# Performance work log

Hardware: AMD Instinct MI355X
Metric: run time of the kernel (lower is better)

Reference implementation:

```python
import jax, jax.numpy as jnp
import numpy as np

N_NODES = 40000
N_EDGES = 640000
HIDDEN = 128


def setup_inputs() -> dict:
    key = jax.random.key(0)
    k1, k2, k3, k4 = jax.random.split(key, 4)
    x = jax.random.normal(k1, (N_NODES, HIDDEN), dtype=jnp.float32)
    edge_index = jax.random.randint(k2, (2, N_EDGES), 0, N_NODES, dtype=jnp.int64)
    # nn.Linear(2*hidden, 1): weight [1, 2*hidden], bias [1]
    bound = 1.0 / np.sqrt(2 * HIDDEN)
    att_w = jax.random.uniform(k3, (1, 2 * HIDDEN), minval=-bound, maxval=bound, dtype=jnp.float32)
    att_b = jax.random.uniform(k4, (1,), minval=-bound, maxval=bound, dtype=jnp.float32)
    eps = jnp.array([0.1], dtype=jnp.float32)
    return {"x": x, "edge_index": edge_index, "att_w": att_w, "att_b": att_b, "eps": eps}


def reference(x, edge_index, att_w, att_b, eps):
    d = x.shape[1]
    row, col = edge_index[0], edge_index[1]
    x_i = x[row]                               # [E, d]
    x_j = x[col]                               # [E, d]
    # att(cat([x_i, x_j])) == x_i @ w_i + x_j @ w_j + b  (avoids materializing concat)
    w = att_w[0]                               # [2d]
    logits = x_i @ w[:d] + x_j @ w[d:] + att_b[0]   # [E]
    alpha = jnp.tanh(logits)
    messages = alpha[:, None] * x_i            # [E, d]
    out = jax.ops.segment_sum(messages, col, num_segments=x.shape[0])  # scatter_add over col
    e = eps[0]
    return e * x + (1.0 - e) * out
```

## Files before the change

kernel.cpp:

```cpp
#include <hip/hip_runtime.h>
#include <hip/hip_fp16.h>
#include <math.h>


#define NHID 128
#define NNODES 40000
#define NEDGES 640000
#define CAP 64

__global__ __launch_bounds__(256) void node_pre_kernel(
    const float* __restrict__ x,
    const float* __restrict__ att_w,
    const float* __restrict__ att_b,
    float* __restrict__ s1,
    float* __restrict__ s2,
    int* __restrict__ cursor) {
    int gid = blockIdx.x * 256 + threadIdx.x;
    if (gid < NNODES) cursor[gid] = 0;

    int node = blockIdx.x * 4 + (threadIdx.x >> 6);
    int lane = threadIdx.x & 63;
    if (node >= NNODES) return;

    float2 xv = ((const float2*)(x + (size_t)node * NHID))[lane];
    float2 w1 = ((const float2*)att_w)[lane];
    float2 w2 = ((const float2*)(att_w + NHID))[lane];

    float p1 = xv.x * w1.x + xv.y * w1.y;
    float p2 = xv.x * w2.x + xv.y * w2.y;
#pragma unroll
    for (int off = 32; off > 0; off >>= 1) {
        p1 += __shfl_down(p1, off, 64);
        p2 += __shfl_down(p2, off, 64);
    }
    if (lane == 0) {
        s1[node] = p1;
        s2[node] = p2 + att_b[0];
    }
}

__global__ __launch_bounds__(256) void bucket_kernel(
    const int* __restrict__ ei,
    const float* __restrict__ s1,
    const float* __restrict__ s2,
    const float* __restrict__ eps,
    int* __restrict__ cursor,
    unsigned* __restrict__ buck) {
    int e = blockIdx.x * 256 + threadIdx.x;
    if (e >= NEDGES) return;
    int r = ei[e];
    int c = ei[NEDGES + e];
    float a = (1.0f - eps[0]) * tanhf(s1[r] + s2[c]);
    int pos = atomicAdd(&cursor[c], 1);
    if (pos < CAP) {
        unsigned short hb = __half_as_ushort(__float2half_rn(a));
        buck[(size_t)c * CAP + pos] = ((unsigned)r << 16) | (unsigned)hb;
    }
}

__global__ __launch_bounds__(256) void gather_kernel(
    const float* __restrict__ x,
    const float* __restrict__ eps,
    const int* __restrict__ cursor,
    const unsigned* __restrict__ buck,
    float* __restrict__ out) {
    int node = blockIdx.x * 4 + (threadIdx.x >> 6);
    int lane = threadIdx.x & 63;
    if (node >= NNODES) return;

    int cnt = cursor[node];
    cnt = (cnt < CAP) ? cnt : CAP;

    unsigned pk = (lane < cnt) ? buck[(size_t)node * CAP + lane] : 0u;

    float2 xv = ((const float2*)(x + (size_t)node * NHID))[lane];
    float e = eps[0];
    float2 acc;
    acc.x = e * xv.x;
    acc.y = e * xv.y;

    int j = 0;
    for (; j + 4 <= cnt; j += 4) {
        unsigned p0 = __shfl(pk, j + 0, 64);
        unsigned p1 = __shfl(pk, j + 1, 64);
        unsigned p2 = __shfl(pk, j + 2, 64);
        unsigned p3 = __shfl(pk, j + 3, 64);
        float2 v0 = ((const float2*)(x + (size_t)(p0 >> 16) * NHID))[lane];
        float2 v1 = ((const float2*)(x + (size_t)(p1 >> 16) * NHID))[lane];
        float2 v2 = ((const float2*)(x + (size_t)(p2 >> 16) * NHID))[lane];
        float2 v3 = ((const float2*)(x + (size_t)(p3 >> 16) * NHID))[lane];
        float a0 = __half2float(__ushort_as_half((unsigned short)(p0 & 0xffffu)));
        float a1 = __half2float(__ushort_as_half((unsigned short)(p1 & 0xffffu)));
        float a2 = __half2float(__ushort_as_half((unsigned short)(p2 & 0xffffu)));
        float a3 = __half2float(__ushort_as_half((unsigned short)(p3 & 0xffffu)));
        acc.x += a0 * v0.x; acc.y += a0 * v0.y;
        acc.x += a1 * v1.x; acc.y += a1 * v1.y;
        acc.x += a2 * v2.x; acc.y += a2 * v2.y;
        acc.x += a3 * v3.x; acc.y += a3 * v3.y;
    }
    for (; j < cnt; j++) {
        unsigned p = __shfl(pk, j, 64);
        float2 v = ((const float2*)(x + (size_t)(p >> 16) * NHID))[lane];
        float a = __half2float(__ushort_as_half((unsigned short)(p & 0xffffu)));
        acc.x += a * v.x;
        acc.y += a * v.y;
    }
    ((float2*)(out + (size_t)node * NHID))[lane] = acc;
}

extern "C" void kernel_launch(void* const* d_in, const int* in_sizes, int n_in,
                              void* d_out, int out_size, void* d_ws, size_t ws_size,
                              hipStream_t stream) {
    const float* x     = (const float*)d_in[0];
    const int*   ei    = (const int*)d_in[1];
    const float* att_w = (const float*)d_in[2];
    const float* att_b = (const float*)d_in[3];
    const float* eps   = (const float*)d_in[4];
    float* out = (float*)d_out;

    float*    s1     = (float*)d_ws;
    float*    s2     = s1 + NNODES;
    int*      cursor = (int*)(s2 + NNODES);
    unsigned* buck   = (unsigned*)(cursor + NNODES);

    node_pre_kernel<<<NNODES / 4, 256, 0, stream>>>(
        x, att_w, att_b, s1, s2, cursor);
    bucket_kernel<<<(NEDGES + 255) / 256, 256, 0, stream>>>(
        ei, s1, s2, eps, cursor, buck);
    gather_kernel<<<NNODES / 4, 256, 0, stream>>>(
        x, eps, cursor, buck, out);
}
```

Measured before the change: 162.1 us.

## Gather fp16 copy of x, defer tanh to gather, pad atomic counters

The pre-pass now writes an fp16 copy of x, and the gather kernel reads neighbour rows from that copy, halving the bytes of the random row gathers. The attention coefficient is no longer computed in the bucket kernel. Buckets hold only 16-bit row indices, and the gather kernel computes tanh per lane from s1/s2 before broadcasting it with shuffles. Per-node counters are spaced 16 ints apart to spread the atomics across cache lines. This adds fp16 rounding of neighbour features, and the 16-bit row index cannot represent node ids above 65535.

```diff
diff --git a/kernel.cpp b/kernel.cpp
--- a/kernel.cpp
+++ b/kernel.cpp
@@ -7,6 +7,7 @@
 #define NNODES 40000
 #define NEDGES 640000
 #define CAP 64
+#define CSTRIDE 16
 
 __global__ __launch_bounds__(256) void node_pre_kernel(
     const float* __restrict__ x,
@@ -14,9 +15,10 @@
     const float* __restrict__ att_b,
     float* __restrict__ s1,
     float* __restrict__ s2,
+    __half* __restrict__ xh,
     int* __restrict__ cursor) {
     int gid = blockIdx.x * 256 + threadIdx.x;
-    if (gid < NNODES) cursor[gid] = 0;
+    if (gid < NNODES * CSTRIDE) cursor[gid] = 0;
 
     int node = blockIdx.x * 4 + (threadIdx.x >> 6);
     int lane = threadIdx.x & 63;
@@ -25,6 +27,11 @@
     float2 xv = ((const float2*)(x + (size_t)node * NHID))[lane];
     float2 w1 = ((const float2*)att_w)[lane];
     float2 w2 = ((const float2*)(att_w + NHID))[lane];
+
+    __half2 hv;
+    hv.x = __float2half_rn(xv.x);
+    hv.y = __float2half_rn(xv.y);
+    ((__half2*)(xh + (size_t)node * NHID))[lane] = hv;
 
     float p1 = xv.x * w1.x + xv.y * w1.y;
     float p2 = xv.x * w2.x + xv.y * w2.y;
@@ -41,67 +48,67 @@
 
 __global__ __launch_bounds__(256) void bucket_kernel(
     const int* __restrict__ ei,
-    const float* __restrict__ s1,
-    const float* __restrict__ s2,
-    const float* __restrict__ eps,
     int* __restrict__ cursor,
-    unsigned* __restrict__ buck) {
+    unsigned short* __restrict__ buck) {
     int e = blockIdx.x * 256 + threadIdx.x;
     if (e >= NEDGES) return;
     int r = ei[e];
     int c = ei[NEDGES + e];
-    float a = (1.0f - eps[0]) * tanhf(s1[r] + s2[c]);
-    int pos = atomicAdd(&cursor[c], 1);
+    int pos = atomicAdd(&cursor[c * CSTRIDE], 1);
     if (pos < CAP) {
-        unsigned short hb = __half_as_ushort(__float2half_rn(a));
-        buck[(size_t)c * CAP + pos] = ((unsigned)r << 16) | (unsigned)hb;
+        buck[(size_t)c * CAP + pos] = (unsigned short)r;
     }
 }
 
 __global__ __launch_bounds__(256) void gather_kernel(
     const float* __restrict__ x,
+    const __half* __restrict__ xh,
+    const float* __restrict__ s1,
+    const float* __restrict__ s2,
     const float* __restrict__ eps,
     const int* __restrict__ cursor,
-    const unsigned* __restrict__ buck,
+    const unsigned short* __restrict__ buck,
     float* __restrict__ out) {
     int node = blockIdx.x * 4 + (threadIdx.x >> 6);
     int lane = threadIdx.x & 63;
     if (node >= NNODES) return;
 
-    int cnt = cursor[node];
+    int cnt = cursor[node * CSTRIDE];
     cnt = (cnt < CAP) ? cnt : CAP;
 
-    unsigned pk = (lane < cnt) ? buck[(size_t)node * CAP + lane] : 0u;
+    float e = eps[0];
+    float coef = 1.0f - e;
+    float s2n = s2[node];
+
+    int   r_l = (lane < cnt) ? (int)buck[(size_t)node * CAP + lane] : 0;
+    float a_l = (lane < cnt) ? coef * tanhf(s1[r_l] + s2n) : 0.0f;
 
     float2 xv = ((const float2*)(x + (size_t)node * NHID))[lane];
-    float e = eps[0];
     float2 acc;
     acc.x = e * xv.x;
     acc.y = e * xv.y;
 
     int j = 0;
     for (; j + 4 <= cnt; j += 4) {
-        unsigned p0 = __shfl(pk, j + 0, 64);
-        unsigned p1 = __shfl(pk, j + 1, 64);
-        unsigned p2 = __shfl(pk, j + 2, 64);
-        unsigned p3 = __shfl(pk, j + 3, 64);
-        float2 v0 = ((const float2*)(x + (size_t)(p0 >> 16) * NHID))[lane];
-        float2 v1 = ((const float2*)(x + (size_t)(p1 >> 16) * NHID))[lane];
-        float2 v2 = ((const float2*)(x + (size_t)(p2 >> 16) * NHID))[lane];
-        float2 v3 = ((const float2*)(x + (size_t)(p3 >> 16) * NHID))[lane];
-        float a0 = __half2float(__ushort_as_half((unsigned short)(p0 & 0xffffu)));
-        float a1 = __half2float(__ushort_as_half((unsigned short)(p1 & 0xffffu)));
-        float a2 = __half2float(__ushort_as_half((unsigned short)(p2 & 0xffffu)));
-        float a3 = __half2float(__ushort_as_half((unsigned short)(p3 & 0xffffu)));
+        int   r0 = __shfl(r_l, j + 0, 64), r1 = __shfl(r_l, j + 1, 64);
+        int   r2 = __shfl(r_l, j + 2, 64), r3 = __shfl(r_l, j + 3, 64);
+        float a0 = __shfl(a_l, j + 0, 64), a1 = __shfl(a_l, j + 1, 64);
+        float a2 = __shfl(a_l, j + 2, 64), a3 = __shfl(a_l, j + 3, 64);
+        __half2 h0 = ((const __half2*)(xh + (size_t)r0 * NHID))[lane];
+        __half2 h1 = ((const __half2*)(xh + (size_t)r1 * NHID))[lane];
+        __half2 h2 = ((const __half2*)(xh + (size_t)r2 * NHID))[lane];
+        __half2 h3 = ((const __half2*)(xh + (size_t)r3 * NHID))[lane];
+        float2 v0 = __half22float2(h0), v1 = __half22float2(h1);
+        float2 v2 = __half22float2(h2), v3 = __half22float2(h3);
         acc.x += a0 * v0.x; acc.y += a0 * v0.y;
         acc.x += a1 * v1.x; acc.y += a1 * v1.y;
         acc.x += a2 * v2.x; acc.y += a2 * v2.y;
         acc.x += a3 * v3.x; acc.y += a3 * v3.y;
     }
     for (; j < cnt; j++) {
-        unsigned p = __shfl(pk, j, 64);
-        float2 v = ((const float2*)(x + (size_t)(p >> 16) * NHID))[lane];
-        float a = __half2float(__ushort_as_half((unsigned short)(p & 0xffffu)));
+        int   r = __shfl(r_l, j, 64);
+        float a = __shfl(a_l, j, 64);
+        float2 v = __half22float2(((const __half2*)(xh + (size_t)r * NHID))[lane]);
         acc.x += a * v.x;
         acc.y += a * v.y;
     }
@@ -118,15 +125,15 @@
     const float* eps   = (const float*)d_in[4];
     float* out = (float*)d_out;
 
-    float*    s1     = (float*)d_ws;
-    float*    s2     = s1 + NNODES;
-    int*      cursor = (int*)(s2 + NNODES);
-    unsigned* buck   = (unsigned*)(cursor + NNODES);
+    float*          s1     = (float*)d_ws;
+    float*          s2     = s1 + NNODES;
+    __half*         xh     = (__half*)(s2 + NNODES);
+    int*            cursor = (int*)(xh + (size_t)NNODES * NHID);
+    unsigned short* buck   = (unsigned short*)(cursor + NNODES * CSTRIDE);
 
     node_pre_kernel<<<NNODES / 4, 256, 0, stream>>>(
-        x, att_w, att_b, s1, s2, cursor);
-    bucket_kernel<<<(NEDGES + 255) / 256, 256, 0, stream>>>(
-        ei, s1, s2, eps, cursor, buck);
+        x, att_w, att_b, s1, s2, xh, cursor);
+    bucket_kernel<<<(NEDGES + 255) / 256, 256, 0, stream>>>(ei, cursor, buck);
     gather_kernel<<<NNODES / 4, 256, 0, stream>>>(
-        x, eps, cursor, buck, out);
+        x, xh, s1, s2, eps, cursor, buck, out);
 }
```

Result: faster. 143.3 us (-11.6%).
